# Kernel optimization log

Hardware: AMD Instinct MI355X
Metric: run time of the kernel (lower is better)

Reference implementation:

```python
import jax, jax.numpy as jnp
import numpy as np

B, H, S, D = 4, 16, 2048, 64


def setup_inputs() -> dict:
    key = jax.random.key(0)
    kq, kk, kv, kp = jax.random.split(key, 4)
    query = jax.random.normal(kq, (B, H, S, D), dtype=jnp.float32)
    k = jax.random.normal(kk, (B, H, S, D), dtype=jnp.float32)
    value = jax.random.normal(kv, (B, H, S, D), dtype=jnp.float32)
    # 0/1 key-padding mask, broadcastable against the [S, S] causal mask
    padding_mask = jax.random.randint(kp, (B, 1, 1, S), 0, 2, dtype=jnp.int32)
    return {"query": query, "key": k, "value": value, "padding_mask": padding_mask}


def reference(query, key, value, padding_mask):
    d_k = query.shape[-1]
    seq_len = query.shape[-2]
    # scores: [B, H, S, S]
    scores = jnp.einsum("bhqd,bhkd->bhqk", query, key) / jnp.sqrt(jnp.float32(d_k))
    # causal mask: 1 above diagonal
    future = jnp.triu(jnp.ones((seq_len, seq_len), dtype=jnp.float32), k=1)
    combined = future + padding_mask.astype(jnp.float32)  # values in {0,1,2}
    # faithful to torch masked_fill(combined_mask == 1, -1e9): only exact 1 is masked
    scores = jnp.where(combined == 1.0, jnp.float32(-1e9), scores)
    attention_weights = jax.nn.softmax(scores, axis=-1)
    result = attention_weights @ value  # [B, H, S, D]
    return result, attention_weights
```

## Files before the change

### kernel.cpp

```cpp
#include <hip/hip_runtime.h>

#define SEQ 2048
#define DH  64
#define NH  16
#define NB  4
#define QT  64
#define NT  512
#define NHEADS (NB * NH)
#define NKT (SEQ / 64)
#define NBLK (NHEADS * (SEQ / QT))
#define TILE_ELEMS 4096

typedef _Float16 f16x8 __attribute__((ext_vector_type(8)));
typedef short    s16x8 __attribute__((ext_vector_type(8)));
typedef float    f32x4 __attribute__((ext_vector_type(4)));

static __device__ __forceinline__ int swe(int row, int col) {
    return (row << 6) + (col ^ ((row & 7) << 3));
}

static __device__ __forceinline__ void gload16(const void* g, void* l) {
    __builtin_amdgcn_global_load_lds(
        (const __attribute__((address_space(1))) void*)g,
        (__attribute__((address_space(3))) void*)l, 16, 0, 0);
}

static __device__ __forceinline__ short f16b(float x) {
    _Float16 h = (_Float16)x;
    return __builtin_bit_cast(short, h);
}

__global__ __launch_bounds__(256) void prep(
    const float* __restrict__ K, const float* __restrict__ V,
    short* __restrict__ kh, short* __restrict__ kl,
    short* __restrict__ vh, short* __restrict__ vl)
{
    const int t    = threadIdx.x;
    const int kt   = blockIdx.x & (NKT - 1);
    const int head = blockIdx.x >> 5;
    const size_t toff = ((size_t)head * NKT + kt) * TILE_ELEMS;
    const float* Kg = K + ((size_t)head * SEQ + (size_t)kt * 64) * DH;
    const float* Vg = V + ((size_t)head * SEQ + (size_t)kt * 64) * DH;

    {
        const int row = t >> 2;
        const int c0  = (t & 3) * 16;
        const float4* gp = (const float4*)(Kg + (size_t)row * DH + c0);
        const float4 v0 = gp[0], v1 = gp[1], v2 = gp[2], v3 = gp[3];
        const float x[16] = {v0.x,v0.y,v0.z,v0.w, v1.x,v1.y,v1.z,v1.w,
                             v2.x,v2.y,v2.z,v2.w, v3.x,v3.y,v3.z,v3.w};
        s16x8 hi[2], lo[2];
#pragma unroll
        for (int j = 0; j < 16; ++j) {
            _Float16 h = (_Float16)x[j];
            hi[j >> 3][j & 7] = __builtin_bit_cast(short, h);
            lo[j >> 3][j & 7] = f16b(x[j] - (float)h);
        }
        *(s16x8*)&kh[toff + swe(row, c0)]     = hi[0];
        *(s16x8*)&kh[toff + swe(row, c0 + 8)] = hi[1];
        *(s16x8*)&kl[toff + swe(row, c0)]     = lo[0];
        *(s16x8*)&kl[toff + swe(row, c0 + 8)] = lo[1];
    }
    {
#pragma unroll
        for (int half = 0; half < 2; ++half) {
            const int d  = t & 63;
            const int k0 = half * 32 + (t >> 6) * 8;
            s16x8 hi8, lo8;
#pragma unroll
            for (int i = 0; i < 8; ++i) {
                float x = Vg[(size_t)(k0 + i) * DH + d];
                _Float16 h = (_Float16)x;
                hi8[i] = __builtin_bit_cast(short, h);
                lo8[i] = f16b(x - (float)h);
            }
            *(s16x8*)&vh[toff + swe(d, k0)] = hi8;
            *(s16x8*)&vl[toff + swe(d, k0)] = lo8;
        }
    }
}

#define QK_TILE(A0, A1) do {                                                         \
  _Pragma("unroll") for (int dh = 0; dh < 2; ++dh) {                                 \
    const int d0 = dh * 32 + lg * 8;                                                 \
    const f16x8 bh = *(const f16x8*)&s_kh[swe(key, d0)];                             \
    const f16x8 bl = *(const f16x8*)&s_kl[swe(key, d0)];                             \
    A0 = __builtin_amdgcn_mfma_f32_16x16x32_f16(qfh[0][dh], bh, A0, 0, 0, 0);        \
    A1 = __builtin_amdgcn_mfma_f32_16x16x32_f16(qfh[1][dh], bh, A1, 0, 0, 0);        \
    A0 = __builtin_amdgcn_mfma_f32_16x16x32_f16(qfh[0][dh], bl, A0, 0, 0, 0);        \
    A1 = __builtin_amdgcn_mfma_f32_16x16x32_f16(qfh[1][dh], bl, A1, 0, 0, 0);        \
    A0 = __builtin_amdgcn_mfma_f32_16x16x32_f16(qfl[0][dh], bh, A0, 0, 0, 0);        \
    A1 = __builtin_amdgcn_mfma_f32_16x16x32_f16(qfl[1][dh], bh, A1, 0, 0, 0);        \
  } } while (0)

__global__ __launch_bounds__(NT, 4) void attn_fwd(
    const float* __restrict__ Q,
    const short* __restrict__ KH, const short* __restrict__ KL,
    const short* __restrict__ VH, const short* __restrict__ VL,
    const int* __restrict__ pad,
    float* __restrict__ out_res, float* __restrict__ out_w)
{
    __shared__ __attribute__((aligned(16))) short s_kh[TILE_ELEMS], s_kl[TILE_ELEMS];
    __shared__ __attribute__((aligned(16))) short s_vh[TILE_ELEMS], s_vl[TILE_ELEMS];
    __shared__ __attribute__((aligned(16))) short s_w [TILE_ELEMS];
    __shared__ __attribute__((aligned(16))) union { short q[2][TILE_ELEMS]; float o[64][68]; } s_u;
    __shared__ float s_red[64][4];

    const int t = threadIdx.x;
    int bid = blockIdx.x;
    bid = (bid & 7) * (NBLK / 8) + (bid >> 3);

    const int qtile = bid & (SEQ / QT - 1);
    const int head  = bid >> 5;
    const int q0    = qtile * QT;
    const size_t hoff = (size_t)head * SEQ * DH;
    const size_t woff = (size_t)head * SEQ * SEQ;
    const int*   padb = pad + (head >> 4) * SEQ;

    const short* khh = KH + (size_t)head * NKT * TILE_ELEMS;
    const short* klh = KL + (size_t)head * NKT * TILE_ELEMS;
    const short* vhh = VH + (size_t)head * NKT * TILE_ELEMS;
    const short* vlh = VL + (size_t)head * NKT * TILE_ELEMS;

    const int l  = t & 63;
    const int w  = t >> 6;
    const int wq = w >> 2;
    const int wk = w & 3;
    const int lj = l & 15;
    const int lg = l >> 4;

    {
        const int row = t >> 3;
        const int c0  = (t & 7) * 8;
        const float* gp = Q + hoff + (size_t)(q0 + row) * DH + c0;
        const float4 a = *(const float4*)gp;
        const float4 b = *(const float4*)(gp + 4);
        const float x[8] = {a.x,a.y,a.z,a.w, b.x,b.y,b.z,b.w};
        s16x8 hi8, lo8;
#pragma unroll
        for (int j = 0; j < 8; ++j) {
            _Float16 h = (_Float16)x[j];
            hi8[j] = __builtin_bit_cast(short, h);
            lo8[j] = f16b(x[j] - (float)h);
        }
        *(s16x8*)&s_u.q[0][swe(row, c0)] = hi8;
        *(s16x8*)&s_u.q[1][swe(row, c0)] = lo8;
    }
    __syncthreads();

    f16x8 qfh[2][2], qfl[2][2];
#pragma unroll
    for (int m = 0; m < 2; ++m)
#pragma unroll
        for (int dh = 0; dh < 2; ++dh) {
            const int row = wq * 32 + m * 16 + lj;
            const int d0  = dh * 32 + lg * 8;
            qfh[m][dh] = *(const f16x8*)&s_u.q[0][swe(row, d0)];
            qfl[m][dh] = *(const f16x8*)&s_u.q[1][swe(row, d0)];
        }

    const int key = wk * 16 + lj;

    float rs[2][4] = {};
#pragma unroll 1
    for (int kt = 0; kt < NKT; ++kt) {
        __syncthreads();
        {
            const size_t off = (size_t)kt * TILE_ELEMS + (size_t)t * 8;
            gload16(khh + off, &s_kh[w * 512]);
            gload16(klh + off, &s_kl[w * 512]);
        }
        __syncthreads();

        f32x4 a0 = {0.f,0.f,0.f,0.f}, a1 = {0.f,0.f,0.f,0.f};
        QK_TILE(a0, a1);

        const int ka = kt * 64 + key;
        const int pd = padb[ka];
#pragma unroll
        for (int m = 0; m < 2; ++m) {
            const f32x4 av = m ? a1 : a0;
            const int qrow = q0 + wq * 32 + m * 16 + lg * 4;
#pragma unroll
            for (int r = 0; r < 4; ++r) {
                const bool msk = ((ka > qrow + r) != (pd == 1));
                const float s  = msk ? -8.0e9f : av[r];
                rs[m][r] += __expf(s * 0.125f);
            }
        }
    }
#pragma unroll
    for (int m = 0; m < 2; ++m)
#pragma unroll
        for (int r = 0; r < 4; ++r) {
            float v = rs[m][r];
#pragma unroll
            for (int off = 1; off < 16; off <<= 1) v += __shfl_xor(v, off, 64);
            rs[m][r] = v;
        }
    if (lj == 0) {
#pragma unroll
        for (int m = 0; m < 2; ++m)
#pragma unroll
            for (int r = 0; r < 4; ++r)
                s_red[wq * 32 + m * 16 + lg * 4 + r][wk] = rs[m][r];
    }
    __syncthreads();
    float invr[2][4];
#pragma unroll
    for (int m = 0; m < 2; ++m)
#pragma unroll
        for (int r = 0; r < 4; ++r) {
            const int row = wq * 32 + m * 16 + lg * 4 + r;
            invr[m][r] = 1.0f / (s_red[row][0] + s_red[row][1] +
                                 s_red[row][2] + s_red[row][3]);
        }

    f32x4 ov[2][2];
#pragma unroll
    for (int m = 0; m < 2; ++m)
#pragma unroll
        for (int n = 0; n < 2; ++n) ov[m][n] = (f32x4){0.f,0.f,0.f,0.f};

    const int wk2   = wk >> 1;
    const int dbase = (wk & 1) * 32;
    const int ks    = wk2 * 32 + lg * 8;

#pragma unroll 1
    for (int kt = 0; kt < NKT; ++kt) {
        __syncthreads();
        {
            const size_t off = (size_t)kt * TILE_ELEMS + (size_t)t * 8;
            gload16(khh + off, &s_kh[w * 512]);
            gload16(klh + off, &s_kl[w * 512]);
            gload16(vhh + off, &s_vh[w * 512]);
            gload16(vlh + off, &s_vl[w * 512]);
        }
        __syncthreads();

        f32x4 a0 = {0.f,0.f,0.f,0.f}, a1 = {0.f,0.f,0.f,0.f};
        QK_TILE(a0, a1);

        const int ka = kt * 64 + key;
        const int pd = padb[ka];
#pragma unroll
        for (int m = 0; m < 2; ++m) {
            const f32x4 av = m ? a1 : a0;
            const int qrowg = q0 + wq * 32 + m * 16 + lg * 4;
            const int qrowl = wq * 32 + m * 16 + lg * 4;
#pragma unroll
            for (int r = 0; r < 4; ++r) {
                const bool msk = ((ka > qrowg + r) != (pd == 1));
                const float s  = msk ? -8.0e9f : av[r];
                const float e  = __expf(s * 0.125f);
                const float wgt = e * invr[m][r];
                out_w[woff + (size_t)(qrowg + r) * SEQ + ka] = wgt;
                s_w[swe(qrowl + r, key)] = f16b(wgt);
            }
        }
        __syncthreads();

        {
            const f16x8 aw0 = *(const f16x8*)&s_w[swe(wq * 32 + lj,      ks)];
            const f16x8 aw1 = *(const f16x8*)&s_w[swe(wq * 32 + 16 + lj, ks)];
            const f16x8 bh0 = *(const f16x8*)&s_vh[swe(dbase + lj,      ks)];
            const f16x8 bh1 = *(const f16x8*)&s_vh[swe(dbase + 16 + lj, ks)];
            const f16x8 bl0 = *(const f16x8*)&s_vl[swe(dbase + lj,      ks)];
            const f16x8 bl1 = *(const f16x8*)&s_vl[swe(dbase + 16 + lj, ks)];
            ov[0][0] = __builtin_amdgcn_mfma_f32_16x16x32_f16(aw0, bh0, ov[0][0], 0,0,0);
            ov[0][1] = __builtin_amdgcn_mfma_f32_16x16x32_f16(aw0, bh1, ov[0][1], 0,0,0);
            ov[1][0] = __builtin_amdgcn_mfma_f32_16x16x32_f16(aw1, bh0, ov[1][0], 0,0,0);
            ov[1][1] = __builtin_amdgcn_mfma_f32_16x16x32_f16(aw1, bh1, ov[1][1], 0,0,0);
            ov[0][0] = __builtin_amdgcn_mfma_f32_16x16x32_f16(aw0, bl0, ov[0][0], 0,0,0);
            ov[0][1] = __builtin_amdgcn_mfma_f32_16x16x32_f16(aw0, bl1, ov[0][1], 0,0,0);
            ov[1][0] = __builtin_amdgcn_mfma_f32_16x16x32_f16(aw1, bl0, ov[1][0], 0,0,0);
            ov[1][1] = __builtin_amdgcn_mfma_f32_16x16x32_f16(aw1, bl1, ov[1][1], 0,0,0);
        }
    }

    if (wk2 == 0) {
#pragma unroll
        for (int m = 0; m < 2; ++m)
#pragma unroll
            for (int n = 0; n < 2; ++n)
#pragma unroll
                for (int r = 0; r < 4; ++r)
                    s_u.o[wq * 32 + m * 16 + lg * 4 + r][dbase + n * 16 + lj] = ov[m][n][r];
    }
    __syncthreads();
    if (wk2 == 1) {
#pragma unroll
        for (int m = 0; m < 2; ++m)
#pragma unroll
            for (int n = 0; n < 2; ++n)
#pragma unroll
                for (int r = 0; r < 4; ++r)
                    s_u.o[wq * 32 + m * 16 + lg * 4 + r][dbase + n * 16 + lj] += ov[m][n][r];
    }
    __syncthreads();
    {
        const int row = t >> 3;
        const int c0  = (t & 7) * 8;
        const float4 v0 = *(const float4*)&s_u.o[row][c0];
        const float4 v1 = *(const float4*)&s_u.o[row][c0 + 4];
        float* op = out_res + hoff + (size_t)(q0 + row) * DH + c0;
        *(float4*)op       = v0;
        *(float4*)(op + 4) = v1;
    }
}

extern "C" void kernel_launch(void* const* d_in, const int* in_sizes, int n_in,
                              void* d_out, int out_size, void* d_ws, size_t ws_size,
                              hipStream_t stream) {
    const float* Q   = (const float*)d_in[0];
    const float* K   = (const float*)d_in[1];
    const float* V   = (const float*)d_in[2];
    const int*   pad = (const int*)d_in[3];
    float* out_res = (float*)d_out;
    float* out_w   = out_res + (size_t)NB * NH * SEQ * DH;

    const size_t T = (size_t)NHEADS * NKT * TILE_ELEMS;
    short* kh = (short*)d_ws;
    short* kl = kh + T;
    short* vh = kl + T;
    short* vl = vh + T;

    prep<<<dim3(NHEADS * NKT), 256, 0, stream>>>(K, V, kh, kl, vh, vl);
    attn_fwd<<<dim3(NBLK), NT, 0, stream>>>(Q, kh, kl, vh, vl, pad, out_res, out_w);
}
```

Before: 1.595 ms.

## Double-buffer K/V tiles, fuse PV into first pass, precompute padding bitmask

The first pass now computes unnormalized exp weights and accumulates P·V together with the row sums. Normalization is applied at the end, and the weights are written out in a final K-only pass. K and V tiles are double-buffered with async global-to-LDS loads and explicit waitcnt barriers, so loads overlap MFMA work, and MFMA sections raise wave priority. The padding mask is packed into per-key bitmasks by the prep kernel to drop a per-tile global load. The price is extra LDS for the double buffers, which may reduce occupancy, and f16 rounding of unnormalized weights in P·V.

```diff
diff --git a/kernel.cpp b/kernel.cpp
--- a/kernel.cpp
+++ b/kernel.cpp
@@ -32,8 +32,10 @@
 
 __global__ __launch_bounds__(256) void prep(
     const float* __restrict__ K, const float* __restrict__ V,
+    const int* __restrict__ pad,
     short* __restrict__ kh, short* __restrict__ kl,
-    short* __restrict__ vh, short* __restrict__ vl)
+    short* __restrict__ vh, short* __restrict__ vl,
+    unsigned* __restrict__ pm)
 {
     const int t    = threadIdx.x;
     const int kt   = blockIdx.x & (NKT - 1);
@@ -78,13 +80,21 @@
             *(s16x8*)&vl[toff + swe(d, k0)] = lo8;
         }
     }
-}
-
-#define QK_TILE(A0, A1) do {                                                         \
+    if (blockIdx.x == 0) {
+        const int b = t >> 6, klc = t & 63;
+        unsigned mword = 0;
+#pragma unroll
+        for (int kt2 = 0; kt2 < NKT; ++kt2)
+            mword |= (unsigned)(pad[b * SEQ + kt2 * 64 + klc] & 1) << kt2;
+        pm[t] = mword;
+    }
+}
+
+#define QK_TILE(kb_, A0, A1) do {                                                    \
   _Pragma("unroll") for (int dh = 0; dh < 2; ++dh) {                                 \
-    const int d0 = dh * 32 + lg * 8;                                                 \
-    const f16x8 bh = *(const f16x8*)&s_kh[swe(key, d0)];                             \
-    const f16x8 bl = *(const f16x8*)&s_kl[swe(key, d0)];                             \
+    const int d0_ = dh * 32 + lg * 8;                                                \
+    const f16x8 bh = *(const f16x8*)&s_k[kb_][0][swe(key, d0_)];                     \
+    const f16x8 bl = *(const f16x8*)&s_k[kb_][1][swe(key, d0_)];                     \
     A0 = __builtin_amdgcn_mfma_f32_16x16x32_f16(qfh[0][dh], bh, A0, 0, 0, 0);        \
     A1 = __builtin_amdgcn_mfma_f32_16x16x32_f16(qfh[1][dh], bh, A1, 0, 0, 0);        \
     A0 = __builtin_amdgcn_mfma_f32_16x16x32_f16(qfh[0][dh], bl, A0, 0, 0, 0);        \
@@ -93,17 +103,37 @@
     A1 = __builtin_amdgcn_mfma_f32_16x16x32_f16(qfl[1][dh], bh, A1, 0, 0, 0);        \
   } } while (0)
 
+#define STAGE_K(buf_, kt_) do {                                                      \
+    const size_t o_ = (size_t)(kt_) * TILE_ELEMS + (size_t)t * 8;                    \
+    gload16(khh + o_, &s_k[buf_][0][w * 512]);                                       \
+    gload16(klh + o_, &s_k[buf_][1][w * 512]);                                       \
+} while (0)
+#define STAGE_V(buf_, kt_) do {                                                      \
+    const size_t o_ = (size_t)(kt_) * TILE_ELEMS + (size_t)t * 8;                    \
+    gload16(vhh + o_, &s_vu.v[buf_][0][w * 512]);                                    \
+    gload16(vlh + o_, &s_vu.v[buf_][1][w * 512]);                                    \
+} while (0)
+
+#define WAIT_BAR(cnt_) do {                                                          \
+    asm volatile("s_waitcnt " cnt_ ::: "memory");                                    \
+    __builtin_amdgcn_s_barrier();                                                    \
+    __builtin_amdgcn_sched_barrier(0);                                               \
+} while (0)
+
 __global__ __launch_bounds__(NT, 4) void attn_fwd(
     const float* __restrict__ Q,
     const short* __restrict__ KH, const short* __restrict__ KL,
     const short* __restrict__ VH, const short* __restrict__ VL,
-    const int* __restrict__ pad,
+    const unsigned* __restrict__ PM,
     float* __restrict__ out_res, float* __restrict__ out_w)
 {
-    __shared__ __attribute__((aligned(16))) short s_kh[TILE_ELEMS], s_kl[TILE_ELEMS];
-    __shared__ __attribute__((aligned(16))) short s_vh[TILE_ELEMS], s_vl[TILE_ELEMS];
-    __shared__ __attribute__((aligned(16))) short s_w [TILE_ELEMS];
-    __shared__ __attribute__((aligned(16))) union { short q[2][TILE_ELEMS]; float o[64][68]; } s_u;
+    __shared__ __attribute__((aligned(16))) short s_k[2][2][TILE_ELEMS];
+    __shared__ union __attribute__((aligned(16))) {
+        short v[2][2][TILE_ELEMS];
+        short q[2][TILE_ELEMS];
+        float o[64][68];
+    } s_vu;
+    __shared__ __attribute__((aligned(16))) short s_w[TILE_ELEMS];
     __shared__ float s_red[64][4];
 
     const int t = threadIdx.x;
@@ -115,7 +145,6 @@
     const int q0    = qtile * QT;
     const size_t hoff = (size_t)head * SEQ * DH;
     const size_t woff = (size_t)head * SEQ * SEQ;
-    const int*   padb = pad + (head >> 4) * SEQ;
 
     const short* khh = KH + (size_t)head * NKT * TILE_ELEMS;
     const short* klh = KL + (size_t)head * NKT * TILE_ELEMS;
@@ -128,6 +157,9 @@
     const int wk = w & 3;
     const int lj = l & 15;
     const int lg = l >> 4;
+
+    const int key = wk * 16 + lj;
+    const unsigned pmask = PM[(head >> 4) * 64 + key];
 
     {
         const int row = t >> 3;
@@ -143,8 +175,8 @@
             hi8[j] = __builtin_bit_cast(short, h);
             lo8[j] = f16b(x[j] - (float)h);
         }
-        *(s16x8*)&s_u.q[0][swe(row, c0)] = hi8;
-        *(s16x8*)&s_u.q[1][swe(row, c0)] = lo8;
+        *(s16x8*)&s_vu.q[0][swe(row, c0)] = hi8;
+        *(s16x8*)&s_vu.q[1][swe(row, c0)] = lo8;
     }
     __syncthreads();
 
@@ -155,118 +187,65 @@
         for (int dh = 0; dh < 2; ++dh) {
             const int row = wq * 32 + m * 16 + lj;
             const int d0  = dh * 32 + lg * 8;
-            qfh[m][dh] = *(const f16x8*)&s_u.q[0][swe(row, d0)];
-            qfl[m][dh] = *(const f16x8*)&s_u.q[1][swe(row, d0)];
-        }
-
-    const int key = wk * 16 + lj;
+            qfh[m][dh] = *(const f16x8*)&s_vu.q[0][swe(row, d0)];
+            qfl[m][dh] = *(const f16x8*)&s_vu.q[1][swe(row, d0)];
+        }
+    asm volatile("s_waitcnt lgkmcnt(0)" ::: "memory");
+    __syncthreads();
+
+    const int wk2   = wk >> 1;
+    const int dbase = (wk & 1) * 32;
+    const int ks    = wk2 * 32 + lg * 8;
 
     float rs[2][4] = {};
+    f32x4 ov[2][2];
+#pragma unroll
+    for (int m = 0; m < 2; ++m)
+#pragma unroll
+        for (int n = 0; n < 2; ++n) ov[m][n] = (f32x4){0.f,0.f,0.f,0.f};
+
+    STAGE_K(0, 0);
+    STAGE_V(0, 0);
+    WAIT_BAR("vmcnt(0)");
+
 #pragma unroll 1
     for (int kt = 0; kt < NKT; ++kt) {
-        __syncthreads();
-        {
-            const size_t off = (size_t)kt * TILE_ELEMS + (size_t)t * 8;
-            gload16(khh + off, &s_kh[w * 512]);
-            gload16(klh + off, &s_kl[w * 512]);
-        }
-        __syncthreads();
+        const int cur = kt & 1, nxt = cur ^ 1;
+        const int ktn = (kt + 1) & (NKT - 1);
+        STAGE_K(nxt, ktn);
+        STAGE_V(nxt, ktn);
 
         f32x4 a0 = {0.f,0.f,0.f,0.f}, a1 = {0.f,0.f,0.f,0.f};
-        QK_TILE(a0, a1);
+        __builtin_amdgcn_s_setprio(1);
+        QK_TILE(cur, a0, a1);
+        __builtin_amdgcn_s_setprio(0);
 
         const int ka = kt * 64 + key;
-        const int pd = padb[ka];
+        const int pd = (int)((pmask >> kt) & 1u);
 #pragma unroll
         for (int m = 0; m < 2; ++m) {
             const f32x4 av = m ? a1 : a0;
             const int qrow = q0 + wq * 32 + m * 16 + lg * 4;
+            const int qloc = wq * 32 + m * 16 + lg * 4;
 #pragma unroll
             for (int r = 0; r < 4; ++r) {
                 const bool msk = ((ka > qrow + r) != (pd == 1));
                 const float s  = msk ? -8.0e9f : av[r];
-                rs[m][r] += __expf(s * 0.125f);
+                const float e  = __expf(s * 0.125f);
+                rs[m][r] += e;
+                s_w[swe(qloc + r, key)] = f16b(e);
             }
         }
-    }
-#pragma unroll
-    for (int m = 0; m < 2; ++m)
-#pragma unroll
-        for (int r = 0; r < 4; ++r) {
-            float v = rs[m][r];
-#pragma unroll
-            for (int off = 1; off < 16; off <<= 1) v += __shfl_xor(v, off, 64);
-            rs[m][r] = v;
-        }
-    if (lj == 0) {
-#pragma unroll
-        for (int m = 0; m < 2; ++m)
-#pragma unroll
-            for (int r = 0; r < 4; ++r)
-                s_red[wq * 32 + m * 16 + lg * 4 + r][wk] = rs[m][r];
-    }
-    __syncthreads();
-    float invr[2][4];
-#pragma unroll
-    for (int m = 0; m < 2; ++m)
-#pragma unroll
-        for (int r = 0; r < 4; ++r) {
-            const int row = wq * 32 + m * 16 + lg * 4 + r;
-            invr[m][r] = 1.0f / (s_red[row][0] + s_red[row][1] +
-                                 s_red[row][2] + s_red[row][3]);
-        }
-
-    f32x4 ov[2][2];
-#pragma unroll
-    for (int m = 0; m < 2; ++m)
-#pragma unroll
-        for (int n = 0; n < 2; ++n) ov[m][n] = (f32x4){0.f,0.f,0.f,0.f};
-
-    const int wk2   = wk >> 1;
-    const int dbase = (wk & 1) * 32;
-    const int ks    = wk2 * 32 + lg * 8;
-
-#pragma unroll 1
-    for (int kt = 0; kt < NKT; ++kt) {
-        __syncthreads();
-        {
-            const size_t off = (size_t)kt * TILE_ELEMS + (size_t)t * 8;
-            gload16(khh + off, &s_kh[w * 512]);
-            gload16(klh + off, &s_kl[w * 512]);
-            gload16(vhh + off, &s_vh[w * 512]);
-            gload16(vlh + off, &s_vl[w * 512]);
-        }
-        __syncthreads();
-
-        f32x4 a0 = {0.f,0.f,0.f,0.f}, a1 = {0.f,0.f,0.f,0.f};
-        QK_TILE(a0, a1);
-
-        const int ka = kt * 64 + key;
-        const int pd = padb[ka];
-#pragma unroll
-        for (int m = 0; m < 2; ++m) {
-            const f32x4 av = m ? a1 : a0;
-            const int qrowg = q0 + wq * 32 + m * 16 + lg * 4;
-            const int qrowl = wq * 32 + m * 16 + lg * 4;
-#pragma unroll
-            for (int r = 0; r < 4; ++r) {
-                const bool msk = ((ka > qrowg + r) != (pd == 1));
-                const float s  = msk ? -8.0e9f : av[r];
-                const float e  = __expf(s * 0.125f);
-                const float wgt = e * invr[m][r];
-                out_w[woff + (size_t)(qrowg + r) * SEQ + ka] = wgt;
-                s_w[swe(qrowl + r, key)] = f16b(wgt);
-            }
-        }
-        __syncthreads();
+        WAIT_BAR("lgkmcnt(0)");
 
         {
             const f16x8 aw0 = *(const f16x8*)&s_w[swe(wq * 32 + lj,      ks)];
             const f16x8 aw1 = *(const f16x8*)&s_w[swe(wq * 32 + 16 + lj, ks)];
-            const f16x8 bh0 = *(const f16x8*)&s_vh[swe(dbase + lj,      ks)];
-            const f16x8 bh1 = *(const f16x8*)&s_vh[swe(dbase + 16 + lj, ks)];
-            const f16x8 bl0 = *(const f16x8*)&s_vl[swe(dbase + lj,      ks)];
-            const f16x8 bl1 = *(const f16x8*)&s_vl[swe(dbase + 16 + lj, ks)];
+            const f16x8 bh0 = *(const f16x8*)&s_vu.v[cur][0][swe(dbase + lj,      ks)];
+            const f16x8 bh1 = *(const f16x8*)&s_vu.v[cur][0][swe(dbase + 16 + lj, ks)];
+            const f16x8 bl0 = *(const f16x8*)&s_vu.v[cur][1][swe(dbase + lj,      ks)];
+            const f16x8 bl1 = *(const f16x8*)&s_vu.v[cur][1][swe(dbase + 16 + lj, ks)];
+            __builtin_amdgcn_s_setprio(1);
             ov[0][0] = __builtin_amdgcn_mfma_f32_16x16x32_f16(aw0, bh0, ov[0][0], 0,0,0);
             ov[0][1] = __builtin_amdgcn_mfma_f32_16x16x32_f16(aw0, bh1, ov[0][1], 0,0,0);
             ov[1][0] = __builtin_amdgcn_mfma_f32_16x16x32_f16(aw1, bh0, ov[1][0], 0,0,0);
@@ -275,8 +254,44 @@
             ov[0][1] = __builtin_amdgcn_mfma_f32_16x16x32_f16(aw0, bl1, ov[0][1], 0,0,0);
             ov[1][0] = __builtin_amdgcn_mfma_f32_16x16x32_f16(aw1, bl0, ov[1][0], 0,0,0);
             ov[1][1] = __builtin_amdgcn_mfma_f32_16x16x32_f16(aw1, bl1, ov[1][1], 0,0,0);
-        }
-    }
+            __builtin_amdgcn_s_setprio(0);
+        }
+        WAIT_BAR("vmcnt(0)");
+    }
+
+#pragma unroll
+    for (int m = 0; m < 2; ++m)
+#pragma unroll
+        for (int r = 0; r < 4; ++r) {
+            float v = rs[m][r];
+#pragma unroll
+            for (int off = 1; off < 16; off <<= 1) v += __shfl_xor(v, off, 64);
+            rs[m][r] = v;
+        }
+    if (lj == 0) {
+#pragma unroll
+        for (int m = 0; m < 2; ++m)
+#pragma unroll
+            for (int r = 0; r < 4; ++r)
+                s_red[wq * 32 + m * 16 + lg * 4 + r][wk] = rs[m][r];
+    }
+    __syncthreads();
+    float invr[2][4];
+#pragma unroll
+    for (int m = 0; m < 2; ++m)
+#pragma unroll
+        for (int r = 0; r < 4; ++r) {
+            const int row = wq * 32 + m * 16 + lg * 4 + r;
+            invr[m][r] = 1.0f / (s_red[row][0] + s_red[row][1] +
+                                 s_red[row][2] + s_red[row][3]);
+        }
+
+#pragma unroll
+    for (int m = 0; m < 2; ++m)
+#pragma unroll
+        for (int n = 0; n < 2; ++n)
+#pragma unroll
+            for (int r = 0; r < 4; ++r) ov[m][n][r] *= invr[m][r];
 
     if (wk2 == 0) {
 #pragma unroll
@@ -285,7 +300,7 @@
             for (int n = 0; n < 2; ++n)
 #pragma unroll
                 for (int r = 0; r < 4; ++r)
-                    s_u.o[wq * 32 + m * 16 + lg * 4 + r][dbase + n * 16 + lj] = ov[m][n][r];
+                    s_vu.o[wq * 32 + m * 16 + lg * 4 + r][dbase + n * 16 + lj] = ov[m][n][r];
     }
     __syncthreads();
     if (wk2 == 1) {
@@ -295,17 +310,44 @@
             for (int n = 0; n < 2; ++n)
 #pragma unroll
                 for (int r = 0; r < 4; ++r)
-                    s_u.o[wq * 32 + m * 16 + lg * 4 + r][dbase + n * 16 + lj] += ov[m][n][r];
+                    s_vu.o[wq * 32 + m * 16 + lg * 4 + r][dbase + n * 16 + lj] += ov[m][n][r];
     }
     __syncthreads();
     {
         const int row = t >> 3;
         const int c0  = (t & 7) * 8;
-        const float4 v0 = *(const float4*)&s_u.o[row][c0];
-        const float4 v1 = *(const float4*)&s_u.o[row][c0 + 4];
+        const float4 v0 = *(const float4*)&s_vu.o[row][c0];
+        const float4 v1 = *(const float4*)&s_vu.o[row][c0 + 4];
         float* op = out_res + hoff + (size_t)(q0 + row) * DH + c0;
         *(float4*)op       = v0;
         *(float4*)(op + 4) = v1;
+    }
+
+#pragma unroll 1
+    for (int kt = 0; kt < NKT; ++kt) {
+        const int cur = kt & 1, nxt = cur ^ 1;
+        STAGE_K(nxt, (kt + 1) & (NKT - 1));
+
+        f32x4 a0 = {0.f,0.f,0.f,0.f}, a1 = {0.f,0.f,0.f,0.f};
+        __builtin_amdgcn_s_setprio(1);
+        QK_TILE(cur, a0, a1);
+        __builtin_amdgcn_s_setprio(0);
+
+        const int ka = kt * 64 + key;
+        const int pd = (int)((pmask >> kt) & 1u);
+#pragma unroll
+        for (int m = 0; m < 2; ++m) {
+            const f32x4 av = m ? a1 : a0;
+            const int qrow = q0 + wq * 32 + m * 16 + lg * 4;
+#pragma unroll
+            for (int r = 0; r < 4; ++r) {
+                const bool msk = ((ka > qrow + r) != (pd == 1));
+                const float s  = msk ? -8.0e9f : av[r];
+                const float e  = __expf(s * 0.125f);
+                out_w[woff + (size_t)(qrow + r) * SEQ + ka] = e * invr[m][r];
+            }
+        }
+        WAIT_BAR("vmcnt(8)");
     }
 }
 
@@ -324,7 +366,8 @@
     short* kl = kh + T;
     short* vh = kl + T;
     short* vl = vh + T;
-
-    prep<<<dim3(NHEADS * NKT), 256, 0, stream>>>(K, V, kh, kl, vh, vl);
-    attn_fwd<<<dim3(NBLK), NT, 0, stream>>>(Q, kh, kl, vh, vl, pad, out_res, out_w);
-}
+    unsigned* pm = (unsigned*)(vl + T);
+
+    prep<<<dim3(NHEADS * NKT), 256, 0, stream>>>(K, V, pad, kh, kl, vh, vl, pm);
+    attn_fwd<<<dim3(NBLK), NT, 0, stream>>>(Q, kh, kl, vh, vl, pm, out_res, out_w);
+}
```

New measurement: 1.466 ms. 8.1% less time.
